# Performance work log

Hardware: AMD Instinct MI355X
Metric: run time of the kernel (lower is better)

Reference implementation:

```python
import jax, jax.numpy as jnp
import numpy as np

N, D, K_POS, K_NEG = 50000, 256, 32, 20
EPS = 1e-15


def setup_inputs() -> dict:
    key = jax.random.key(0)
    k1, k2, k3, k4, k5 = jax.random.split(key, 5)
    embeddings = jax.random.normal(k1, (N, D), dtype=jnp.float32)
    neighbors_array = jax.random.randint(k2, (N, K_POS), 0, N, dtype=jnp.int32)
    # 0/1 validity mask standing in for the NaN padding of the original float array;
    # force >=1 valid neighbor per row (rows in real data with mask_array==1 have neighbors)
    nbr_mask = jax.random.randint(k3, (N, K_POS), 0, 2, dtype=jnp.int32).at[:, 0].set(1)
    negative_array = jax.random.randint(k4, (N, K_NEG), 0, N, dtype=jnp.int32)
    mask_array = jax.random.randint(k5, (N,), 0, 2, dtype=jnp.int32)
    return {
        "embeddings": embeddings,
        "neighbors_array": neighbors_array,
        "nbr_mask": nbr_mask,
        "negative_array": negative_array,
        "mask_array": mask_array,
    }


def reference(embeddings, neighbors_array, nbr_mask, negative_array, mask_array):
    # Batched ragged gather + dot: dots[n,k] = <emb[nbr[n,k]], emb[n]>
    pos_dots = jnp.einsum("nkd,nd->nk", embeddings[neighbors_array], embeddings)
    neg_dots = jnp.einsum("nkd,nd->nk", embeddings[negative_array], embeddings)

    m = nbr_mask.astype(embeddings.dtype)          # [N, K_pos] validity (NaN filter)
    cnt = m.sum(-1)                                # valid-neighbor count per row

    pos_term = -jnp.log(jax.nn.sigmoid(pos_dots) + EPS)          # [N, K_pos]
    pos_loss = (pos_term * m).sum(-1) / jnp.maximum(cnt, 1.0)    # masked mean
    # Rows with zero valid neighbors produce NaN in the original (mean of empty)
    pos_loss = jnp.where(cnt > 0, pos_loss, jnp.nan)

    neg_loss = (-jnp.log(1.0 - jax.nn.sigmoid(neg_dots) + EPS)).mean(-1)  # [N]

    row_loss = pos_loss + neg_loss
    # original skips NaN rows (adds 0) but still divides by sum(mask_array)
    row_loss = jnp.where(jnp.isnan(row_loss), 0.0, row_loss)

    rmask = mask_array.astype(embeddings.dtype)
    return (row_loss * rmask).sum() / rmask.sum()
```

## Files before the change

kernel.cpp:

```cpp
#include <hip/hip_runtime.h>
#include <hip/hip_fp16.h>
#include <string.h>

namespace {
constexpr int kN = 50000;
constexpr int kD = 256;
constexpr int kPos = 32;
constexpr int kNeg = 20;
constexpr float kEps = 1e-15f;
constexpr int kSlots = kPos / 4 + kNeg / 4;

typedef float floatx2 __attribute__((ext_vector_type(2)));

#if __has_builtin(__builtin_amdgcn_cvt_pk_f32_fp8)
constexpr bool kHwCvtPk = true;
constexpr bool kHwCvt1 = false;
#elif __has_builtin(__builtin_amdgcn_cvt_f32_fp8)
constexpr bool kHwCvtPk = false;
constexpr bool kHwCvt1 = true;
#else
constexpr bool kHwCvtPk = false;
constexpr bool kHwCvt1 = false;
#endif
constexpr float kOwnScale = (kHwCvtPk || kHwCvt1) ? 1.f : 256.f;

__device__ __forceinline__ uint enc1(float x) {
    const __half hh = __float2half(x * 0.00390625f);
    unsigned short t;
    memcpy(&t, &hh, 2);
    const uint s = ((uint)t >> 8) & 0x80u;
    uint mag = (uint)t & 0x7fffu;
    mag = mag + 0x3fu + ((mag >> 7) & 1u);
    uint u = mag >> 7;
    if (u > 0x7eu) u = 0x7eu;
    return s | u;
}

__device__ __forceinline__ float dec_h(uint h) {
    __half hh;
    const unsigned short t = (unsigned short)h;
    memcpy(&hh, &t, 2);
    return __half2float(hh);
}

__device__ __forceinline__ void dq4f(uint u, const float4& o, float& d) {
#if __has_builtin(__builtin_amdgcn_cvt_pk_f32_fp8)
    const floatx2 lo = __builtin_amdgcn_cvt_pk_f32_fp8((int)u, false);
    const floatx2 hi = __builtin_amdgcn_cvt_pk_f32_fp8((int)u, true);
    d = fmaf(lo.x, o.x, d);
    d = fmaf(lo.y, o.y, d);
    d = fmaf(hi.x, o.z, d);
    d = fmaf(hi.y, o.w, d);
#elif __has_builtin(__builtin_amdgcn_cvt_f32_fp8)
    d = fmaf(__builtin_amdgcn_cvt_f32_fp8((int)u, 0), o.x, d);
    d = fmaf(__builtin_amdgcn_cvt_f32_fp8((int)u, 1), o.y, d);
    d = fmaf(__builtin_amdgcn_cvt_f32_fp8((int)u, 2), o.z, d);
    d = fmaf(__builtin_amdgcn_cvt_f32_fp8((int)u, 3), o.w, d);
#else
    const float v0 = dec_h(((u << 8) & 0x8000u) | ((u << 7) & 0x3f80u));
    const float v1 = dec_h((u & 0x8000u) | ((u >> 1) & 0x3f80u));
    const float v2 = dec_h(((u >> 8) & 0x8000u) | ((u >> 9) & 0x3f80u));
    const float v3 = dec_h(((u >> 16) & 0x8000u) | ((u >> 17) & 0x3f80u));
    d = fmaf(v0, o.x, d);
    d = fmaf(v1, o.y, d);
    d = fmaf(v2, o.z, d);
    d = fmaf(v3, o.w, d);
#endif
}

__global__ __launch_bounds__(256) void convert_fp8(const float* __restrict__ emb,
                                                   uint* __restrict__ tbl) {
    const size_t i = ((size_t)blockIdx.x * 256 + threadIdx.x) * 8;
    const float4* src = reinterpret_cast<const float4*>(emb + i);
    const float4 a = src[0];
    const float4 b = src[1];
    uint2 o;
    o.x = enc1(a.x) | (enc1(a.y) << 8) | (enc1(a.z) << 16) | (enc1(a.w) << 24);
    o.y = enc1(b.x) | (enc1(b.y) << 8) | (enc1(b.z) << 16) | (enc1(b.w) << 24);
    reinterpret_cast<uint2*>(tbl)[i / 8] = o;
}

__global__ __launch_bounds__(256) void compact_kernel(const int* __restrict__ rmask,
                                                      int* __restrict__ list,
                                                      float* __restrict__ acc) {
    const int n = blockIdx.x * 256 + threadIdx.x;
    if (n < kN && rmask[n]) {
        const int p = atomicAdd(reinterpret_cast<unsigned*>(&acc[2]), 1u);
        list[p] = n;
    }
}

__global__ __launch_bounds__(256) void row_loss_fp8(
    const float* __restrict__ emb,
    const uchar* __restrict__ tblb,
    const int* __restrict__ nbr,
    const int* __restrict__ nbrm,
    const int* __restrict__ neg,
    const int* __restrict__ list,
    float* __restrict__ acc) {
    __shared__ float s_num[4];
    const int wave = threadIdx.x >> 6;
    const int lane = threadIdx.x & 63;
    const int g = lane >> 4;
    const int t = lane & 15;

    const int cnt_active = reinterpret_cast<const int*>(acc)[2];
    const int i = blockIdx.x * 4 + wave;
    float num = 0.f;

    if (i < cnt_active) {
        const int n = list[i];

        const float4* erow = reinterpret_cast<const float4*>(emb + (size_t)n * kD);
        float4 own4[4];
#pragma unroll
        for (int q = 0; q < 4; ++q) {
            const float4 f = erow[16 * q + t];
            own4[q].x = f.x * kOwnScale;
            own4[q].y = f.y * kOwnScale;
            own4[q].z = f.z * kOwnScale;
            own4[q].w = f.w * kOwnScale;
        }

        const int* nrow = nbr + (size_t)n * kPos;
        const int* mrow = nbrm + (size_t)n * kPos;
        const int* grow = neg + (size_t)n * kNeg;

        uint offb[kSlots];
        float w[kPos / 4];
        float cnt = 0.f;
#pragma unroll
        for (int s = 0; s < kPos / 4; ++s) {
            offb[s] = (uint)nrow[s * 4 + g] << 8;
            const float mf = (float)mrow[s * 4 + g];
            w[s] = mf;
            cnt += mf;
        }
#pragma unroll
        for (int s = 0; s < kNeg / 4; ++s)
            offb[kPos / 4 + s] = (uint)grow[s * 4 + g] << 8;

        float dlane[kSlots];
#pragma unroll
        for (int s = 0; s < kSlots; ++s) dlane[s] = 0.f;

        const uchar* tbl_t = tblb + 4u * (uint)t;
#pragma unroll
        for (int q = 0; q < 4; ++q) {
            uint u[kSlots];
#pragma unroll
            for (int s = 0; s < kSlots; ++s)
                u[s] = *reinterpret_cast<const uint*>(tbl_t + offb[s] + 64u * (uint)q);
#pragma unroll
            for (int s = 0; s < kSlots; ++s) dq4f(u[s], own4[q], dlane[s]);
        }

        float pos_sum = 0.f, neg_sum = 0.f;
#pragma unroll
        for (int s = 0; s < kSlots; ++s) {
            float d = dlane[s];
            d += __shfl_xor(d, 8);
            d += __shfl_xor(d, 4);
            d += __shfl_xor(d, 2);
            d += __shfl_xor(d, 1);
            const float sg = 1.f / (1.f + __expf(-d));
            if (s < kPos / 4) {
                pos_sum += -__logf(sg + kEps) * w[s];
            } else {
                neg_sum += -__logf(1.f - sg + kEps);
            }
        }

        pos_sum += __shfl_xor(pos_sum, 16);
        pos_sum += __shfl_xor(pos_sum, 32);
        neg_sum += __shfl_xor(neg_sum, 16);
        neg_sum += __shfl_xor(neg_sum, 32);
        cnt += __shfl_xor(cnt, 16);
        cnt += __shfl_xor(cnt, 32);

        if (cnt > 0.f) num = pos_sum / cnt + neg_sum / (float)kNeg;
    }

    if (lane == 0) s_num[wave] = num;
    __syncthreads();
    if (threadIdx.x == 0) {
        const float v = s_num[0] + s_num[1] + s_num[2] + s_num[3];
        if (v != 0.f) atomicAdd(&acc[0], v);
    }
}

__global__ void finalize_kernel(const float* __restrict__ acc, float* __restrict__ out) {
    out[0] = acc[0] / (float)reinterpret_cast<const int*>(acc)[2];
}

__global__ __launch_bounds__(256) void row_loss_f32(
    const float* __restrict__ emb,
    const int* __restrict__ nbr,
    const int* __restrict__ nbrm,
    const int* __restrict__ neg,
    const int* __restrict__ rmask,
    float* __restrict__ acc) {
    __shared__ float s_num[4];
    __shared__ float s_den[4];
    const int wave = threadIdx.x >> 6;
    const int lane = threadIdx.x & 63;
    const int n = blockIdx.x * 4 + wave;
    const int g = lane >> 4;
    const int t = lane & 15;

    const float4* erow = reinterpret_cast<const float4*>(emb + (size_t)n * kD);
    float4 own4[4];
#pragma unroll
    for (int j = 0; j < 4; ++j) own4[j] = erow[j * 16 + t];

    const int* nrow = nbr + (size_t)n * kPos;
    const int* mrow = nbrm + (size_t)n * kPos;
    const int* grow = neg + (size_t)n * kNeg;

    float pos_sum = 0.f, neg_sum = 0.f, cnt = 0.f;
#pragma unroll
    for (int it = 0; it < kPos / 4; ++it) {
        const int idx = nrow[it * 4 + g];
        const float mf = (float)mrow[it * 4 + g];
        cnt += mf;
        const float4* brow = reinterpret_cast<const float4*>(emb + (size_t)idx * kD);
        float d = 0.f;
#pragma unroll
        for (int j = 0; j < 4; ++j) {
            const float4 b = brow[j * 16 + t];
            const float4 a = own4[j];
            d += a.x * b.x + a.y * b.y + a.z * b.z + a.w * b.w;
        }
        d += __shfl_xor(d, 8);
        d += __shfl_xor(d, 4);
        d += __shfl_xor(d, 2);
        d += __shfl_xor(d, 1);
        const float s = 1.f / (1.f + __expf(-d));
        pos_sum += -__logf(s + kEps) * mf;
    }
#pragma unroll
    for (int it = 0; it < kNeg / 4; ++it) {
        const int idx = grow[it * 4 + g];
        const float4* brow = reinterpret_cast<const float4*>(emb + (size_t)idx * kD);
        float d = 0.f;
#pragma unroll
        for (int j = 0; j < 4; ++j) {
            const float4 b = brow[j * 16 + t];
            const float4 a = own4[j];
            d += a.x * b.x + a.y * b.y + a.z * b.z + a.w * b.w;
        }
        d += __shfl_xor(d, 8);
        d += __shfl_xor(d, 4);
        d += __shfl_xor(d, 2);
        d += __shfl_xor(d, 1);
        const float s = 1.f / (1.f + __expf(-d));
        neg_sum += -__logf(1.f - s + kEps);
    }

    pos_sum += __shfl_xor(pos_sum, 16);
    pos_sum += __shfl_xor(pos_sum, 32);
    neg_sum += __shfl_xor(neg_sum, 16);
    neg_sum += __shfl_xor(neg_sum, 32);
    cnt += __shfl_xor(cnt, 16);
    cnt += __shfl_xor(cnt, 32);

    float num = 0.f;
    if (cnt > 0.f) num = pos_sum / cnt + neg_sum / (float)kNeg;
    const float rmf = (float)rmask[n];

    if (lane == 0) {
        s_num[wave] = num * rmf;
        s_den[wave] = rmf;
    }
    __syncthreads();
    if (threadIdx.x == 0) {
        atomicAdd(&acc[0], s_num[0] + s_num[1] + s_num[2] + s_num[3]);
        atomicAdd(&acc[1], s_den[0] + s_den[1] + s_den[2] + s_den[3]);
    }
}

__global__ void finalize_f32(const float* __restrict__ acc, float* __restrict__ out) {
    out[0] = acc[0] / acc[1];
}
}

extern "C" void kernel_launch(void* const* d_in, const int* in_sizes, int n_in,
                              void* d_out, int out_size, void* d_ws, size_t ws_size,
                              hipStream_t stream) {
    const float* emb = (const float*)d_in[0];
    const int* nbr = (const int*)d_in[1];
    const int* nbrm = (const int*)d_in[2];
    const int* neg = (const int*)d_in[3];
    const int* rmask = (const int*)d_in[4];
    float* acc = (float*)d_ws;

    const size_t tbl_bytes = (size_t)kN * kD;
    const size_t list_bytes = (size_t)kN * sizeof(int);
    if (ws_size >= 256 + tbl_bytes + list_bytes) {
        uint* tbl = (uint*)((char*)d_ws + 256);
        int* list = (int*)((char*)d_ws + 256 + tbl_bytes);
        hipMemsetAsync(acc, 0, 4 * sizeof(float), stream);
        compact_kernel<<<(kN + 255) / 256, 256, 0, stream>>>(rmask, list, acc);
        convert_fp8<<<kN * kD / 8 / 256, 256, 0, stream>>>(emb, tbl);
        row_loss_fp8<<<(kN + 3) / 4, 256, 0, stream>>>(emb, (const uchar*)tbl, nbr,
                                                       nbrm, neg, list, acc);
        finalize_kernel<<<1, 1, 0, stream>>>(acc, (float*)d_out);
    } else {
        hipMemsetAsync(acc, 0, 2 * sizeof(float), stream);
        row_loss_f32<<<kN / 4, 256, 0, stream>>>(emb, nbr, nbrm, neg, rmask, acc);
        finalize_f32<<<1, 1, 0, stream>>>(acc, (float*)d_out);
    }
}
```

Baseline: 204.2 us.

## Gather fp8 rows with dwordx4 loads and overlap dot products via staged waitcnt

Each lane now reads 16 contiguous fp8 bytes per neighbor row with a single global_load_dwordx4, replacing four strided 4-byte loads, and the own-row layout is remapped to match. All 13 gathers are issued up front through inline asm, then each slot waits with a decreasing vmcnt so its dot product and loss math run while later loads are still in flight. This is meant to cut the number of memory instructions and hide gather latency. The hand-written waitcnt and asm loads rely on the compiler not inserting other vector-memory operations in between, which makes the code fragile.

```diff
diff --git a/kernel.cpp b/kernel.cpp
--- a/kernel.cpp
+++ b/kernel.cpp
@@ -11,6 +11,7 @@
 constexpr int kSlots = kPos / 4 + kNeg / 4;
 
 typedef float floatx2 __attribute__((ext_vector_type(2)));
+typedef uint uintx4 __attribute__((ext_vector_type(4)));
 
 #if __has_builtin(__builtin_amdgcn_cvt_pk_f32_fp8)
 constexpr bool kHwCvtPk = true;
@@ -68,6 +69,19 @@
 #endif
 }
 
+__device__ __forceinline__ float dot16(const uintx4 u, const float4* o) {
+    float d = 0.f;
+    dq4f(u[0], o[0], d);
+    dq4f(u[1], o[1], d);
+    dq4f(u[2], o[2], d);
+    dq4f(u[3], o[3], d);
+    d += __shfl_xor(d, 8);
+    d += __shfl_xor(d, 4);
+    d += __shfl_xor(d, 2);
+    d += __shfl_xor(d, 1);
+    return d;
+}
+
 __global__ __launch_bounds__(256) void convert_fp8(const float* __restrict__ emb,
                                                    uint* __restrict__ tbl) {
     const size_t i = ((size_t)blockIdx.x * 256 + threadIdx.x) * 8;
@@ -114,62 +128,69 @@
         const float4* erow = reinterpret_cast<const float4*>(emb + (size_t)n * kD);
         float4 own4[4];
 #pragma unroll
-        for (int q = 0; q < 4; ++q) {
-            const float4 f = erow[16 * q + t];
-            own4[q].x = f.x * kOwnScale;
-            own4[q].y = f.y * kOwnScale;
-            own4[q].z = f.z * kOwnScale;
-            own4[q].w = f.w * kOwnScale;
+        for (int j = 0; j < 4; ++j) {
+            const float4 f = erow[4 * t + j];
+            own4[j].x = f.x * kOwnScale;
+            own4[j].y = f.y * kOwnScale;
+            own4[j].z = f.z * kOwnScale;
+            own4[j].w = f.w * kOwnScale;
         }
 
         const int* nrow = nbr + (size_t)n * kPos;
         const int* mrow = nbrm + (size_t)n * kPos;
         const int* grow = neg + (size_t)n * kNeg;
 
-        uint offb[kSlots];
+        uint off[kSlots];
         float w[kPos / 4];
         float cnt = 0.f;
 #pragma unroll
         for (int s = 0; s < kPos / 4; ++s) {
-            offb[s] = (uint)nrow[s * 4 + g] << 8;
+            off[s] = ((uint)nrow[s * 4 + g] << 8) + (uint)t * 16u;
             const float mf = (float)mrow[s * 4 + g];
             w[s] = mf;
             cnt += mf;
         }
 #pragma unroll
         for (int s = 0; s < kNeg / 4; ++s)
-            offb[kPos / 4 + s] = (uint)grow[s * 4 + g] << 8;
-
-        float dlane[kSlots];
-#pragma unroll
-        for (int s = 0; s < kSlots; ++s) dlane[s] = 0.f;
-
-        const uchar* tbl_t = tblb + 4u * (uint)t;
-#pragma unroll
-        for (int q = 0; q < 4; ++q) {
-            uint u[kSlots];
-#pragma unroll
-            for (int s = 0; s < kSlots; ++s)
-                u[s] = *reinterpret_cast<const uint*>(tbl_t + offb[s] + 64u * (uint)q);
-#pragma unroll
-            for (int s = 0; s < kSlots; ++s) dq4f(u[s], own4[q], dlane[s]);
-        }
+            off[kPos / 4 + s] = ((uint)grow[s * 4 + g] << 8) + (uint)t * 16u;
+
+        asm volatile("s_waitcnt vmcnt(0)" ::: "memory");
+        __builtin_amdgcn_sched_barrier(0);
+
+        uintx4 uc[kSlots];
+#define LOADS(s)                                                           \
+    asm volatile("global_load_dwordx4 %0, %1, %2"                          \
+                 : "=&v"(uc[s])                                            \
+                 : "v"(off[s]), "s"(tblb)                                  \
+                 : "memory")
+        LOADS(0); LOADS(1); LOADS(2); LOADS(3); LOADS(4); LOADS(5);
+        LOADS(6); LOADS(7); LOADS(8); LOADS(9); LOADS(10); LOADS(11);
+        LOADS(12);
+#undef LOADS
 
         float pos_sum = 0.f, neg_sum = 0.f;
-#pragma unroll
-        for (int s = 0; s < kSlots; ++s) {
-            float d = dlane[s];
-            d += __shfl_xor(d, 8);
-            d += __shfl_xor(d, 4);
-            d += __shfl_xor(d, 2);
-            d += __shfl_xor(d, 1);
-            const float sg = 1.f / (1.f + __expf(-d));
-            if (s < kPos / 4) {
-                pos_sum += -__logf(sg + kEps) * w[s];
-            } else {
-                neg_sum += -__logf(1.f - sg + kEps);
-            }
-        }
+#define PSLOT(s, nw)                                                       \
+    do {                                                                   \
+        asm volatile("s_waitcnt vmcnt(" #nw ")" ::: "memory");             \
+        __builtin_amdgcn_sched_barrier(0);                                 \
+        const float d = dot16(uc[s], own4);                                \
+        const float sg = 1.f / (1.f + __expf(-d));                         \
+        pos_sum += -__logf(sg + kEps) * w[s];                              \
+    } while (0)
+#define NSLOT(s, nw)                                                       \
+    do {                                                                   \
+        asm volatile("s_waitcnt vmcnt(" #nw ")" ::: "memory");             \
+        __builtin_amdgcn_sched_barrier(0);                                 \
+        const float d = dot16(uc[s], own4);                                \
+        const float sg = 1.f / (1.f + __expf(-d));                         \
+        neg_sum += -__logf(1.f - sg + kEps);                               \
+    } while (0)
+        PSLOT(0, 12); PSLOT(1, 11); PSLOT(2, 10); PSLOT(3, 9);
+        PSLOT(4, 8);  PSLOT(5, 7);  PSLOT(6, 6);  PSLOT(7, 5);
+        NSLOT(8, 4);  NSLOT(9, 3);  NSLOT(10, 2); NSLOT(11, 1);
+        NSLOT(12, 0);
+#undef PSLOT
+#undef NSLOT
 
         pos_sum += __shfl_xor(pos_sum, 16);
         pos_sum += __shfl_xor(pos_sum, 32);
```

After: 202.7 us. About the same (-0.7%).
